# Kernel tuning notes

Measured on AMD Instinct MI355X. Metric: run time of the kernel, lower is better.

The kernel has to match this reference:

```python
import jax, jax.numpy as jnp
import numpy as np

NEG_INF = -1e9

def setup_inputs() -> dict:
    key = jax.random.key(0)
    kq, kk, kv, kt, km = jax.random.split(key, 5)
    B, H, S, D = 2, 16, 2048, 64
    query = jax.random.normal(kq, (B, H, S, D), dtype=jnp.float32)
    k_ = jax.random.normal(kk, (B, H, S, D), dtype=jnp.float32)
    value = jax.random.normal(kv, (B, H, S, D), dtype=jnp.float32)
    time = jax.random.normal(kt, (B, H, S, D), dtype=jnp.float32)
    mask = jax.random.randint(km, (B, 1, S, S), 0, 2, dtype=jnp.int32)
    return {"query": query, "key": k_, "value": value, "time": time, "mask": mask}

def reference(query, key, value, time, mask):
    # scores = (Q K^T + Q T^T) / sqrt(D)  == Q (K+T)^T / sqrt(D)
    scale = 1.0 / jnp.sqrt(jnp.asarray(query.shape[-1], query.dtype))
    query_time = jnp.einsum('bhqd,bhkd->bhqk', query, time) * scale
    query_key = jnp.einsum('bhqd,bhkd->bhqk', query, key) * scale
    scores = query_time + query_key
    scores = jnp.where(mask == 0, jnp.asarray(NEG_INF, scores.dtype), scores)
    p_attn = jax.nn.softmax(scores, axis=-1)
    out = jnp.einsum('bhqk,bhkd->bhqd', p_attn, value)
    return (out, p_attn)
```

## Files before the change

### kernel.cpp

```cpp
#include <hip/hip_runtime.h>
#include <hip/hip_bf16.h>

#define TA_B 2
#define TA_H 16
#define TA_S 2048
#define TA_D 64
#define KTILE 64
#define QB 64
#define NKT (TA_S / KTILE)

typedef __attribute__((ext_vector_type(4))) float f32x4;
typedef __attribute__((ext_vector_type(8))) short bf16x8;
typedef __attribute__((ext_vector_type(8))) unsigned short u16x8;

union BF8 { u16x8 u; bf16x8 s; };

__device__ __forceinline__ unsigned short f2bf(float f) {
    union { float f; unsigned int i; } v; v.f = f;
    unsigned int x = v.i;
    unsigned int r = x + 0x7FFFu + ((x >> 16) & 1u);
    return (unsigned short)(r >> 16);
}

__device__ __forceinline__ void barrier_lds() {
    asm volatile("s_waitcnt lgkmcnt(0)" ::: "memory");
    __builtin_amdgcn_sched_barrier(0);
    __builtin_amdgcn_s_barrier();
    __builtin_amdgcn_sched_barrier(0);
}

__global__ __launch_bounds__(256) void pack_mask(const int* __restrict__ M,
                                                 unsigned long long* __restrict__ Mp) {
    const int nw = TA_B * TA_S * NKT;
    const int wavesTotal = (gridDim.x * blockDim.x) >> 6;
    const int wid  = (blockIdx.x * blockDim.x + threadIdx.x) >> 6;
    const int lane = threadIdx.x & 63;
    for (int w = wid; w < nw; w += wavesTotal) {
        int mv = M[(long)w * 64 + lane];
        unsigned long long bits = __ballot(mv != 0);
        if (lane == 0) Mp[w] = bits;
    }
}

template <bool PACKED>
__global__ __launch_bounds__(256, 4) void ta_fused(
    const float* __restrict__ Qg,
    const float* __restrict__ Kg,
    const float* __restrict__ Vg,
    const float* __restrict__ Tg,
    const int* __restrict__ Mg,
    const unsigned long long* __restrict__ Mp,
    float* __restrict__ Og,
    float* __restrict__ Pg)
{
    __shared__ unsigned short sKp[KTILE][72];
    __shared__ unsigned short sVt[TA_D][72];
    __shared__ unsigned short sP[QB][72];

    const int tid  = threadIdx.x;
    const int wave = tid >> 6;
    const int lane = tid & 63;
    const int c    = lane & 15;
    const int g    = lane >> 4;
    const int row0 = tid >> 3;
    const int cg   = (tid & 7) * 8;

    const int did = blockIdx.x + 32 * (blockIdx.y + 16 * blockIdx.z);
    const int wid = (did & 7) * 128 + (did >> 3);
    const int q0  = (wid & 31) * QB;
    const int h   = (wid >> 5) & 15;
    const int b   = wid >> 9;

    const long bh    = (long)b * TA_H + h;
    const long xBase = bh * (long)TA_S * TA_D;
    const long pBase = bh * (long)TA_S * TA_S;
    const long mBase = (long)b * (long)TA_S * TA_S;
    const int  wq0   = wave * 16;

    bf16x8 qf0, qf1;
    {
        const float* qp = Qg + xBase + (long)(q0 + wq0 + c) * TA_D + g * 8;
        f32x4 a0 = *(const f32x4*)(qp);
        f32x4 a1 = *(const f32x4*)(qp + 4);
        f32x4 b0 = *(const f32x4*)(qp + 32);
        f32x4 b1 = *(const f32x4*)(qp + 36);
        BF8 u0, u1;
#pragma unroll
        for (int i = 0; i < 4; ++i) {
            u0.u[i]     = f2bf(a0[i] * 0.125f);
            u0.u[i + 4] = f2bf(a1[i] * 0.125f);
            u1.u[i]     = f2bf(b0[i] * 0.125f);
            u1.u[i + 4] = f2bf(b1[i] * 0.125f);
        }
        qf0 = u0.s; qf1 = u1.s;
    }

    f32x4 kA0, kA1, tA0, tA1, kB0, kB1, tB0, tB1, vA0, vA1, vB0, vB1;

    auto loadKT = [&](int kt) {
        const long o0 = xBase + (long)(kt * KTILE + row0) * TA_D + cg;
        const long o1 = o0 + 32 * TA_D;
        kA0 = *(const f32x4*)(Kg + o0); kA1 = *(const f32x4*)(Kg + o0 + 4);
        tA0 = *(const f32x4*)(Tg + o0); tA1 = *(const f32x4*)(Tg + o0 + 4);
        kB0 = *(const f32x4*)(Kg + o1); kB1 = *(const f32x4*)(Kg + o1 + 4);
        tB0 = *(const f32x4*)(Tg + o1); tB1 = *(const f32x4*)(Tg + o1 + 4);
    };
    auto loadV = [&](int kt) {
        const long o0 = xBase + (long)(kt * KTILE + row0) * TA_D + cg;
        const long o1 = o0 + 32 * TA_D;
        vA0 = *(const f32x4*)(Vg + o0); vA1 = *(const f32x4*)(Vg + o0 + 4);
        vB0 = *(const f32x4*)(Vg + o1); vB1 = *(const f32x4*)(Vg + o1 + 4);
    };
    auto storeKp = [&]() {
        u16x8 r0, r1;
#pragma unroll
        for (int i = 0; i < 4; ++i) {
            r0[i]     = f2bf(kA0[i] + tA0[i]);
            r0[i + 4] = f2bf(kA1[i] + tA1[i]);
            r1[i]     = f2bf(kB0[i] + tB0[i]);
            r1[i + 4] = f2bf(kB1[i] + tB1[i]);
        }
        *(u16x8*)&sKp[row0][cg]      = r0;
        *(u16x8*)&sKp[row0 + 32][cg] = r1;
    };
    auto storeVt = [&]() {
        const int kpA = row0 ^ cg;
        const int kpB = (row0 + 32) ^ cg;
#pragma unroll
        for (int i = 0; i < 4; ++i) {
            sVt[cg + i][kpA]     = f2bf(vA0[i]);
            sVt[cg + i + 4][kpA] = f2bf(vA1[i]);
            sVt[cg + i][kpB]     = f2bf(vB0[i]);
            sVt[cg + i + 4][kpB] = f2bf(vB1[i]);
        }
    };

    auto maskBits = [&](int kt, int r, float* mb) {
        const int mq = q0 + wq0 + g * 4 + r;
        if constexpr (PACKED) {
            const unsigned long long w = Mp[((long)b * TA_S + mq) * NKT + kt];
            const unsigned lo = (unsigned)w, hi = (unsigned)(w >> 32);
            mb[0] = ((lo >> c) & 1u)        ? 1.0f : 0.0f;
            mb[1] = ((lo >> (16 + c)) & 1u) ? 1.0f : 0.0f;
            mb[2] = ((hi >> c) & 1u)        ? 1.0f : 0.0f;
            mb[3] = ((hi >> (16 + c)) & 1u) ? 1.0f : 0.0f;
        } else {
            const int* mp = Mg + mBase + (long)mq * TA_S + kt * KTILE;
#pragma unroll
            for (int ct = 0; ct < 4; ++ct) mb[ct] = mp[ct * 16 + c] ? 1.0f : 0.0f;
        }
    };

    float lpart[4] = {0.0f, 0.0f, 0.0f, 0.0f};
    loadKT(0);
    for (int kt = 0; kt < NKT; ++kt) {
        storeKp();
        loadKT(kt + 1 < NKT ? kt + 1 : 0);
        barrier_lds();

        f32x4 acc[4];
#pragma unroll
        for (int ct = 0; ct < 4; ++ct)
#pragma unroll
            for (int j = 0; j < 4; ++j) acc[ct][j] = 0.0f;

        __builtin_amdgcn_s_setprio(1);
#pragma unroll
        for (int kk = 0; kk < 2; ++kk) {
            bf16x8 qa = kk ? qf1 : qf0;
#pragma unroll
            for (int ct = 0; ct < 4; ++ct) {
                BF8 bf; bf.u = *(const u16x8*)&sKp[ct * 16 + c][kk * 32 + g * 8];
                acc[ct] = __builtin_amdgcn_mfma_f32_16x16x32_bf16(qa, bf.s, acc[ct], 0, 0, 0);
            }
        }
        __builtin_amdgcn_s_setprio(0);

#pragma unroll
        for (int r = 0; r < 4; ++r) {
            float mb[4];
            maskBits(kt, r, mb);
#pragma unroll
            for (int ct = 0; ct < 4; ++ct)
                lpart[r] += mb[ct] * __expf(acc[ct][r]);
        }
        barrier_lds();
    }

    loadV(0);

    float invl[4];
#pragma unroll
    for (int r = 0; r < 4; ++r) {
        float l = lpart[r];
#pragma unroll
        for (int off = 1; off < 16; off <<= 1)
            l += __shfl_xor(l, off);
        invl[r] = (l > 0.0f) ? (1.0f / l) : 0.0f;
    }

    f32x4 oacc[4];
#pragma unroll
    for (int dt = 0; dt < 4; ++dt)
#pragma unroll
        for (int j = 0; j < 4; ++j) oacc[dt][j] = 0.0f;

    for (int kt = 0; kt < NKT; ++kt) {
        storeKp();
        storeVt();
        const int ktn = kt + 1 < NKT ? kt + 1 : 0;
        loadKT(ktn);
        loadV(ktn);
        barrier_lds();

        f32x4 acc[4];
#pragma unroll
        for (int ct = 0; ct < 4; ++ct)
#pragma unroll
            for (int j = 0; j < 4; ++j) acc[ct][j] = 0.0f;

        __builtin_amdgcn_s_setprio(1);
#pragma unroll
        for (int kk = 0; kk < 2; ++kk) {
            bf16x8 qa = kk ? qf1 : qf0;
#pragma unroll
            for (int ct = 0; ct < 4; ++ct) {
                BF8 bf; bf.u = *(const u16x8*)&sKp[ct * 16 + c][kk * 32 + g * 8];
                acc[ct] = __builtin_amdgcn_mfma_f32_16x16x32_bf16(qa, bf.s, acc[ct], 0, 0, 0);
            }
        }
        __builtin_amdgcn_s_setprio(0);

#pragma unroll
        for (int r = 0; r < 4; ++r) {
            const int mq = q0 + wq0 + g * 4 + r;
            float* pp = Pg + pBase + (long)mq * TA_S + kt * KTILE;
            float mb[4];
            maskBits(kt, r, mb);
#pragma unroll
            for (int ct = 0; ct < 4; ++ct) {
                float e = mb[ct] * __expf(acc[ct][r]);
                __builtin_nontemporal_store(e * invl[r], pp + ct * 16 + c);
                sP[wq0 + g * 4 + r][ct * 16 + c] = f2bf(e);
            }
        }

        BF8 pa0, pa1;
        pa0.u = *(const u16x8*)&sP[wq0 + c][g * 8];
        pa1.u = *(const u16x8*)&sP[wq0 + c][32 + g * 8];
        __builtin_amdgcn_s_setprio(1);
#pragma unroll
        for (int dt = 0; dt < 4; ++dt) {
            const int dRow = dt * 16 + c;
            const int kc0 = (g * 8) ^ (dRow & 56);
            const int kc1 = (32 + g * 8) ^ (dRow & 56);
            BF8 bv0, bv1;
            bv0.u = *(const u16x8*)&sVt[dRow][kc0];
            oacc[dt] = __builtin_amdgcn_mfma_f32_16x16x32_bf16(pa0.s, bv0.s, oacc[dt], 0, 0, 0);
            bv1.u = *(const u16x8*)&sVt[dRow][kc1];
            oacc[dt] = __builtin_amdgcn_mfma_f32_16x16x32_bf16(pa1.s, bv1.s, oacc[dt], 0, 0, 0);
        }
        __builtin_amdgcn_s_setprio(0);

        barrier_lds();
    }

#pragma unroll
    for (int dt = 0; dt < 4; ++dt) {
#pragma unroll
        for (int r = 0; r < 4; ++r) {
            __builtin_nontemporal_store(
                oacc[dt][r] * invl[r],
                &Og[xBase + (long)(q0 + wq0 + g * 4 + r) * TA_D + dt * 16 + c]);
        }
    }
}

extern "C" void kernel_launch(void* const* d_in, const int* in_sizes, int n_in,
                              void* d_out, int out_size, void* d_ws, size_t ws_size,
                              hipStream_t stream) {
    const float* Q = (const float*)d_in[0];
    const float* K = (const float*)d_in[1];
    const float* V = (const float*)d_in[2];
    const float* T = (const float*)d_in[3];
    const int*   M = (const int*)d_in[4];

    float* O = (float*)d_out;
    float* P = O + (long)TA_B * TA_H * TA_S * TA_D;

    unsigned long long* Mp = (unsigned long long*)d_ws;
    const size_t needWs = (size_t)TA_B * TA_S * NKT * sizeof(unsigned long long);

    dim3 grid(TA_S / QB, TA_H, TA_B);
    dim3 block(256);

    if (ws_size >= needWs) {
        hipLaunchKernelGGL(pack_mask, dim3(512), dim3(256), 0, stream, M, Mp);
        hipLaunchKernelGGL(ta_fused<true>, grid, block, 0, stream, Q, K, V, T, M, Mp, O, P);
    } else {
        hipLaunchKernelGGL(ta_fused<false>, grid, block, 0, stream, Q, K, V, T, M, Mp, O, P);
    }
}
```

Measured before the change: 226.1 us.

## Double query block per CTA and vectorize P stores via swizzled LDS

Query rows per block go from 64 to 128 and threads from 256 to 512 (8 waves), so each staged K+T and V tile serves twice as many queries and each thread loads half as much per tile. The normalized probabilities now go to LDS as bf16 under an XOR swizzle, then are read back and written to global as 16-byte vector stores instead of scalar stores. Because P is normalized before the PV MFMA, the final output no longer multiplies by invl. The cost is that the returned P_attn now carries bf16 precision, which is a real loss versus the fp32 stores it replaces. Doubling the block also raises LDS and register pressure per CTA.

```diff
diff --git a/kernel.cpp b/kernel.cpp
--- a/kernel.cpp
+++ b/kernel.cpp
@@ -6,12 +6,14 @@
 #define TA_S 2048
 #define TA_D 64
 #define KTILE 64
-#define QB 64
+#define QB 128
+#define BLOCK 512
 #define NKT (TA_S / KTILE)
 
 typedef __attribute__((ext_vector_type(4))) float f32x4;
 typedef __attribute__((ext_vector_type(8))) short bf16x8;
 typedef __attribute__((ext_vector_type(8))) unsigned short u16x8;
+typedef __attribute__((ext_vector_type(4))) unsigned short u16x4;
 
 union BF8 { u16x8 u; bf16x8 s; };
 
@@ -20,6 +22,9 @@
     unsigned int x = v.i;
     unsigned int r = x + 0x7FFFu + ((x >> 16) & 1u);
     return (unsigned short)(r >> 16);
+}
+__device__ __forceinline__ float bf2f(unsigned short u) {
+    union { unsigned int i; float f; } v; v.i = ((unsigned int)u) << 16; return v.f;
 }
 
 __device__ __forceinline__ void barrier_lds() {
@@ -43,7 +48,7 @@
 }
 
 template <bool PACKED>
-__global__ __launch_bounds__(256, 4) void ta_fused(
+__global__ __launch_bounds__(BLOCK, 4) void ta_fused(
     const float* __restrict__ Qg,
     const float* __restrict__ Kg,
     const float* __restrict__ Vg,
@@ -65,11 +70,11 @@
     const int row0 = tid >> 3;
     const int cg   = (tid & 7) * 8;
 
-    const int did = blockIdx.x + 32 * (blockIdx.y + 16 * blockIdx.z);
-    const int wid = (did & 7) * 128 + (did >> 3);
-    const int q0  = (wid & 31) * QB;
-    const int h   = (wid >> 5) & 15;
-    const int b   = wid >> 9;
+    const int did = blockIdx.x + 16 * (blockIdx.y + 16 * blockIdx.z);
+    const int wid = (did & 7) * 64 + (did >> 3);
+    const int q0  = (wid & 15) * QB;
+    const int h   = (wid >> 4) & 15;
+    const int b   = wid >> 8;
 
     const long bh    = (long)b * TA_H + h;
     const long xBase = bh * (long)TA_S * TA_D;
@@ -95,43 +100,32 @@
         qf0 = u0.s; qf1 = u1.s;
     }
 
-    f32x4 kA0, kA1, tA0, tA1, kB0, kB1, tB0, tB1, vA0, vA1, vB0, vB1;
+    f32x4 kA0, kA1, tA0, tA1, vA0, vA1;
 
     auto loadKT = [&](int kt) {
         const long o0 = xBase + (long)(kt * KTILE + row0) * TA_D + cg;
-        const long o1 = o0 + 32 * TA_D;
         kA0 = *(const f32x4*)(Kg + o0); kA1 = *(const f32x4*)(Kg + o0 + 4);
         tA0 = *(const f32x4*)(Tg + o0); tA1 = *(const f32x4*)(Tg + o0 + 4);
-        kB0 = *(const f32x4*)(Kg + o1); kB1 = *(const f32x4*)(Kg + o1 + 4);
-        tB0 = *(const f32x4*)(Tg + o1); tB1 = *(const f32x4*)(Tg + o1 + 4);
     };
     auto loadV = [&](int kt) {
         const long o0 = xBase + (long)(kt * KTILE + row0) * TA_D + cg;
-        const long o1 = o0 + 32 * TA_D;
         vA0 = *(const f32x4*)(Vg + o0); vA1 = *(const f32x4*)(Vg + o0 + 4);
-        vB0 = *(const f32x4*)(Vg + o1); vB1 = *(const f32x4*)(Vg + o1 + 4);
     };
     auto storeKp = [&]() {
-        u16x8 r0, r1;
+        u16x8 r0;
 #pragma unroll
         for (int i = 0; i < 4; ++i) {
             r0[i]     = f2bf(kA0[i] + tA0[i]);
             r0[i + 4] = f2bf(kA1[i] + tA1[i]);
-            r1[i]     = f2bf(kB0[i] + tB0[i]);
-            r1[i + 4] = f2bf(kB1[i] + tB1[i]);
-        }
-        *(u16x8*)&sKp[row0][cg]      = r0;
-        *(u16x8*)&sKp[row0 + 32][cg] = r1;
+        }
+        *(u16x8*)&sKp[row0][cg] = r0;
     };
     auto storeVt = [&]() {
-        const int kpA = row0 ^ cg;
-        const int kpB = (row0 + 32) ^ cg;
+        const int kp = row0 ^ cg;
 #pragma unroll
         for (int i = 0; i < 4; ++i) {
-            sVt[cg + i][kpA]     = f2bf(vA0[i]);
-            sVt[cg + i + 4][kpA] = f2bf(vA1[i]);
-            sVt[cg + i][kpB]     = f2bf(vB0[i]);
-            sVt[cg + i + 4][kpB] = f2bf(vB1[i]);
+            sVt[cg + i][kp]     = f2bf(vA0[i]);
+            sVt[cg + i + 4][kp] = f2bf(vA1[i]);
         }
     };
 
@@ -233,21 +227,21 @@
 
 #pragma unroll
         for (int r = 0; r < 4; ++r) {
-            const int mq = q0 + wq0 + g * 4 + r;
-            float* pp = Pg + pBase + (long)mq * TA_S + kt * KTILE;
             float mb[4];
             maskBits(kt, r, mb);
 #pragma unroll
             for (int ct = 0; ct < 4; ++ct) {
                 float e = mb[ct] * __expf(acc[ct][r]);
-                __builtin_nontemporal_store(e * invl[r], pp + ct * 16 + c);
-                sP[wq0 + g * 4 + r][ct * 16 + c] = f2bf(e);
+                sP[wq0 + g * 4 + r][((ct ^ r) << 4) + c] = f2bf(e * invl[r]);
             }
         }
 
         BF8 pa0, pa1;
-        pa0.u = *(const u16x8*)&sP[wq0 + c][g * 8];
-        pa1.u = *(const u16x8*)&sP[wq0 + c][32 + g * 8];
+        {
+            const int m = c & 3;
+            pa0.u = *(const u16x8*)&sP[wq0 + c][(((g >> 1) ^ m) << 4) + ((g & 1) << 3)];
+            pa1.u = *(const u16x8*)&sP[wq0 + c][(((2 | (g >> 1)) ^ m) << 4) + ((g & 1) << 3)];
+        }
         __builtin_amdgcn_s_setprio(1);
 #pragma unroll
         for (int dt = 0; dt < 4; ++dt) {
@@ -262,6 +256,19 @@
         }
         __builtin_amdgcn_s_setprio(0);
 
+#pragma unroll
+        for (int j = 0; j < 4; ++j) {
+            const int prow = 4 * j + (g & 3);
+            const int L0   = c * 4;
+            const int phys = (L0 & 12) + ((((L0 >> 4) ^ (prow & 3)) << 4));
+            u16x4 pv = *(const u16x4*)&sP[wq0 + prow][phys];
+            f32x4 v;
+#pragma unroll
+            for (int i = 0; i < 4; ++i) v[i] = bf2f(pv[i]);
+            __builtin_nontemporal_store(
+                v, (f32x4*)(Pg + pBase + (long)(q0 + wq0 + prow) * TA_S + kt * KTILE + L0));
+        }
+
         barrier_lds();
     }
 
@@ -270,7 +277,7 @@
 #pragma unroll
         for (int r = 0; r < 4; ++r) {
             __builtin_nontemporal_store(
-                oacc[dt][r] * invl[r],
+                oacc[dt][r],
                 &Og[xBase + (long)(q0 + wq0 + g * 4 + r) * TA_D + dt * 16 + c]);
         }
     }
@@ -292,7 +299,7 @@
     const size_t needWs = (size_t)TA_B * TA_S * NKT * sizeof(unsigned long long);
 
     dim3 grid(TA_S / QB, TA_H, TA_B);
-    dim3 block(256);
+    dim3 block(BLOCK);
 
     if (ws_size >= needWs) {
         hipLaunchKernelGGL(pack_mask, dim3(512), dim3(256), 0, stream, M, Mp);
```

Result: faster. 194.2 us (-14.1%).
